# Optimization experiments

Measured on AMD Instinct MI355X. Metric: run time of the kernel, lower is better.

Reference implementation:

```python
import jax, jax.numpy as jnp
import numpy as np

N = 50000      # nodes
E = 800000     # edges (before self-loops)
F_IN = 256
H = 4          # heads
C1 = 128
C2 = 64
NCLS = 50
NEG_SLOPE = 0.2


def setup_inputs() -> dict:
    key = jax.random.key(0)
    ks = jax.random.split(key, 12)
    x = jax.random.normal(ks[0], (N, F_IN), dtype=jnp.float32)
    edge_index = jax.random.randint(ks[1], (2, E), 0, N, dtype=jnp.int32)
    s1 = 1.0 / np.sqrt(F_IN)
    s2 = 1.0 / np.sqrt(H * C1)
    s3 = 1.0 / np.sqrt(H * C2)
    return {
        "x": x,
        "edge_index": edge_index,
        "W1": jax.random.normal(ks[2], (F_IN, H * C1), dtype=jnp.float32) * s1,
        "a_src1": jax.random.normal(ks[3], (H, C1), dtype=jnp.float32) * s2,
        "a_dst1": jax.random.normal(ks[4], (H, C1), dtype=jnp.float32) * s2,
        "b1": jnp.zeros((H * C1,), dtype=jnp.float32),
        "W2": jax.random.normal(ks[5], (H * C1, H * C2), dtype=jnp.float32) * s2,
        "a_src2": jax.random.normal(ks[6], (H, C2), dtype=jnp.float32) * s3,
        "a_dst2": jax.random.normal(ks[7], (H, C2), dtype=jnp.float32) * s3,
        "b2": jnp.zeros((H * C2,), dtype=jnp.float32),
        "Wf": jax.random.normal(ks[8], (H * C2, NCLS), dtype=jnp.float32) * s3,
        "bf": jnp.zeros((NCLS,), dtype=jnp.float32),
    }


def _gat_conv(x, src, dst, W, a_src, a_dst, b, heads, ch):
    # h: [N, H, C] transformed features
    h = (x @ W).reshape(N, heads, ch)
    # per-node attention halves (standard GAT decomposition, avoids per-edge d-dim gather for scores)
    asrc = jnp.sum(h * a_src[None], axis=-1)  # [N, H]
    adst = jnp.sum(h * a_dst[None], axis=-1)  # [N, H]
    e = jax.nn.leaky_relu(asrc[src] + adst[dst], NEG_SLOPE)  # [E, H]
    # softmax over edges sharing the same destination node
    m = jax.ops.segment_max(e, dst, num_segments=N)          # [N, H]
    ex = jnp.exp(e - m[dst])
    denom = jax.ops.segment_sum(ex, dst, num_segments=N)     # [N, H]
    alpha = ex / (denom[dst] + 1e-16)                        # [E, H]
    msg = h[src] * alpha[:, :, None]                         # [E, H, C]
    out = jax.ops.segment_sum(msg, dst, num_segments=N)      # [N, H, C]
    return out.reshape(N, heads * ch) + b


def reference(x, edge_index, W1, a_src1, a_dst1, b1, W2, a_src2, a_dst2, b2, Wf, bf):
    # PyG GATConv adds self-loops by default
    loops = jnp.arange(N, dtype=edge_index.dtype)
    src = jnp.concatenate([edge_index[0], loops])
    dst = jnp.concatenate([edge_index[1], loops])
    h = _gat_conv(x, src, dst, W1, a_src1, a_dst1, b1, H, C1)
    h = jax.nn.elu(h)
    # F.dropout is identity in eval mode
    h = _gat_conv(h, src, dst, W2, a_src2, a_dst2, b2, H, C2)
    h = jax.nn.elu(h)
    return h @ Wf + bf
```

## Files before the change

kernel.cpp:

```cpp
#include <hip/hip_runtime.h>
#include <hip/hip_fp16.h>
#include <cmath>

#define NN 50000
#define EE 800000
#define ET 850000
#define HH 4
#define CC1 128
#define CC2 64
#define FIN 256
#define NCLS 50

typedef _Float16 half8_t __attribute__((ext_vector_type(8)));
typedef __attribute__((ext_vector_type(4))) float floatx4;

typedef const __attribute__((address_space(1))) unsigned int* glds_gp_t;
typedef __attribute__((address_space(3))) unsigned int* glds_lp_t;
__device__ __forceinline__ void glds16(const void* g, void* l) {
    __builtin_amdgcn_global_load_lds((glds_gp_t)g, (glds_lp_t)l, 16, 0, 0);
}

#define NB_CAST 12500
#define NB_W1   512
#define NB_W2   512
#define NB_WF   64
#define NB_VA   1
#define NB_HIST 3321
__global__ __launch_bounds__(256) void prep_hist(
    const float* __restrict__ x, __half* __restrict__ xb,
    const float* __restrict__ W1, __half* __restrict__ W1t,
    const float* __restrict__ W2, __half* __restrict__ W2t,
    const float* __restrict__ Wf, __half* __restrict__ Wft,
    const float* __restrict__ a_src1, const float* __restrict__ a_dst1,
    float* __restrict__ va, float* __restrict__ vd,
    const int* __restrict__ ei, int* __restrict__ deg)
{
    int b = blockIdx.x;
    if (b < NB_CAST) {
        int t = b * 256 + threadIdx.x;
        float4 v = *(const float4*)(x + 4 * (size_t)t);
        __half2 p[2];
        p[0] = __floats2half2_rn(v.x, v.y);
        p[1] = __floats2half2_rn(v.z, v.w);
        *(uint2*)(xb + 4 * (size_t)t) = *(uint2*)p;
    } else if (b < NB_CAST + NB_W1) {
        int t = (b - NB_CAST) * 256 + threadIdx.x;
        int n = t >> 8, k = t & 255;
        W1t[t] = __float2half(W1[(size_t)k * 512 + n]);
    } else if (b < NB_CAST + NB_W1 + NB_W2) {
        int t = (b - NB_CAST - NB_W1) * 256 + threadIdx.x;
        int n = t >> 9, k = t & 511;
        W2t[t] = __float2half(W2[(size_t)k * 256 + n]);
    } else if (b < NB_CAST + NB_W1 + NB_W2 + NB_WF) {
        int t = (b - NB_CAST - NB_W1 - NB_W2) * 256 + threadIdx.x;
        int n = t >> 8, k = t & 255;
        Wft[t] = (n < NCLS) ? __float2half(Wf[(size_t)k * NCLS + n]) : __float2half(0.f);
    } else if (b < NB_CAST + NB_W1 + NB_W2 + NB_WF + NB_VA) {
        int k = threadIdx.x;
        const float* wrow = W1 + (size_t)k * 512;
        float s1[4], s2[4];
        #pragma unroll
        for (int h = 0; h < 4; ++h) {
            float a1 = 0.f, a2 = 0.f;
            for (int c = 0; c < 128; ++c) {
                float w = wrow[h * 128 + c];
                a1 += w * a_src1[h * 128 + c];
                a2 += w * a_dst1[h * 128 + c];
            }
            s1[h] = a1; s2[h] = a2;
        }
        *(float4*)(va + 4 * k) = make_float4(s1[0], s1[1], s1[2], s1[3]);
        *(float4*)(vd + 4 * k) = make_float4(s2[0], s2[1], s2[2], s2[3]);
    } else {
        int t = (b - NB_CAST - NB_W1 - NB_W2 - NB_WF - NB_VA) * 256 + threadIdx.x;
        if (t < ET) {
            int dst = (t < EE) ? ei[EE + t] : (t - EE);
            atomicAdd(&deg[dst], 1);
        }
    }
}

#define SCAN_NB 25
__global__ __launch_bounds__(256) void scan_fused(
    const int* __restrict__ deg, int* __restrict__ off, int* __restrict__ pos)
{
    __shared__ int ws[4];
    __shared__ int base_s;
    int tid = threadIdx.x;
    int lane = tid & 63, wid = tid >> 6;

    int lim = blockIdx.x * 2048;
    int s0 = 0;
    for (int i = tid; i < lim; i += 256) s0 += deg[i];
    #pragma unroll
    for (int o = 32; o > 0; o >>= 1) s0 += __shfl_xor(s0, o, 64);
    if (lane == 0) ws[wid] = s0;
    __syncthreads();
    if (tid == 0) base_s = ws[0] + ws[1] + ws[2] + ws[3];
    __syncthreads();
    int base = base_s;
    __syncthreads();

    int i0 = blockIdx.x * 2048 + tid * 8;
    int v[8]; int s = 0;
    #pragma unroll
    for (int k = 0; k < 8; ++k) {
        int i = i0 + k;
        v[k] = (i < NN) ? deg[i] : 0;
        s += v[k];
    }
    int sc = s;
    #pragma unroll
    for (int o = 1; o < 64; o <<= 1) {
        int t = __shfl_up(sc, o, 64);
        if (lane >= o) sc += t;
    }
    if (lane == 63) ws[wid] = sc;
    __syncthreads();
    int woff = base;
    for (int w = 0; w < wid; ++w) woff += ws[w];
    int excl = woff + sc - s;
    #pragma unroll
    for (int k = 0; k < 8; ++k) {
        int i = i0 + k;
        if (i < NN) { off[i] = excl; pos[i] = excl; }
        excl += v[k];
    }
    if (blockIdx.x == 0 && tid == 0) off[NN] = ET;
}

__global__ void edge_scatter(const int* __restrict__ ei,
                             int* __restrict__ pos, int* __restrict__ csr_src)
{
    int t = blockIdx.x * blockDim.x + threadIdx.x;
    if (t >= ET) return;
    int src, dst;
    if (t < EE) { src = ei[t]; dst = ei[EE + t]; }
    else        { src = t - EE; dst = t - EE; }
    int p = atomicAdd(&pos[dst], 1);
    csr_src[p] = src;
}

__global__ __launch_bounds__(256) void attn1x(
    const __half* __restrict__ xb, const float* __restrict__ va,
    const float* __restrict__ vd, float* __restrict__ asrc,
    float* __restrict__ adst)
{
    int wave = threadIdx.x >> 6;
    int lane = threadIdx.x & 63;
    int n = blockIdx.x * 4 + wave;
    if (n >= NN) return;
    int k0 = lane * 4;
    union { uint2 u; __half2 h2[2]; } X;
    X.u = *(const uint2*)(xb + (size_t)n * 256 + k0);
    float xv[4];
    float2 f0 = __half22float2(X.h2[0]);
    float2 f1 = __half22float2(X.h2[1]);
    xv[0] = f0.x; xv[1] = f0.y; xv[2] = f1.x; xv[3] = f1.y;

    float s1[4] = {0.f, 0.f, 0.f, 0.f};
    float s2[4] = {0.f, 0.f, 0.f, 0.f};
    #pragma unroll
    for (int j = 0; j < 4; ++j) {
        float4 a = *(const float4*)(va + 4 * (k0 + j));
        float4 d = *(const float4*)(vd + 4 * (k0 + j));
        s1[0] += xv[j] * a.x; s1[1] += xv[j] * a.y;
        s1[2] += xv[j] * a.z; s1[3] += xv[j] * a.w;
        s2[0] += xv[j] * d.x; s2[1] += xv[j] * d.y;
        s2[2] += xv[j] * d.z; s2[3] += xv[j] * d.w;
    }
    #pragma unroll
    for (int o = 32; o > 0; o >>= 1) {
        #pragma unroll
        for (int h = 0; h < 4; ++h) {
            s1[h] += __shfl_xor(s1[h], o, 64);
            s2[h] += __shfl_xor(s2[h], o, 64);
        }
    }
    if (lane == 0) {
        *(float4*)(asrc + (size_t)n * HH) = make_float4(s1[0], s1[1], s1[2], s1[3]);
        *(float4*)(adst + (size_t)n * HH) = make_float4(s2[0], s2[1], s2[2], s2[3]);
    }
}

__global__ __launch_bounds__(256) void aggregate_x(
    const __half* __restrict__ xb, const int* __restrict__ off,
    const int* __restrict__ csr_src, const float* __restrict__ asrc,
    const float* __restrict__ adst, __half* __restrict__ xagg)
{
    constexpr int UNR = 8;
    __shared__ unsigned int exlds_all[4][64 * 4];
    int wave = threadIdx.x >> 6;
    int lane = threadIdx.x & 63;
    int n = blockIdx.x * 4 + wave;
    if (n >= NN) return;
    unsigned int* exlds = exlds_all[wave];
    int coff = lane * 4;

    int start = off[n], end = off[n + 1];
    float4 advv = *(const float4*)(adst + (size_t)n * HH);
    float dh0 = 0.f, dh1 = 0.f, dh2 = 0.f, dh3 = 0.f;
    __half2 acc2[4][2] = {};

    for (int cb = start; cb < end; cb += 64) {
        int eidx = cb + lane;
        bool valid = eidx < end;
        int s_lane = csr_src[valid ? eidx : end - 1];
        float4 t = *(const float4*)(asrc + (size_t)s_lane * HH);
        float e0 = t.x + advv.x; e0 = e0 > 0.f ? e0 : 0.2f * e0;
        float e1 = t.y + advv.y; e1 = e1 > 0.f ? e1 : 0.2f * e1;
        float e2 = t.z + advv.z; e2 = e2 > 0.f ? e2 : 0.2f * e2;
        float e3 = t.w + advv.w; e3 = e3 > 0.f ? e3 : 0.2f * e3;
        float x0 = valid ? __expf(e0) : 0.f;
        float x1 = valid ? __expf(e1) : 0.f;
        float x2 = valid ? __expf(e2) : 0.f;
        float x3 = valid ? __expf(e3) : 0.f;
        dh0 += x0; dh1 += x1; dh2 += x2; dh3 += x3;
        __half2 xp[4];
        xp[0] = __float2half2_rn(x0);
        xp[1] = __float2half2_rn(x1);
        xp[2] = __float2half2_rn(x2);
        xp[3] = __float2half2_rn(x3);
        *(uint4*)&exlds[lane * 4] = *(uint4*)xp;

        int cnt = end - cb; if (cnt > 64) cnt = 64;
        int jmax = (cnt + UNR - 1) & ~(UNR - 1);
        for (int jj = 0; jj < jmax; jj += UNR) {
            int sidx[UNR]; uint2 uv[UNR];
            #pragma unroll
            for (int u = 0; u < UNR; ++u) {
                sidx[u] = __builtin_amdgcn_readlane(s_lane, jj + u);
                uv[u] = *(const uint2*)(xb + (size_t)sidx[u] * 256 + coff);
            }
            #pragma unroll
            for (int u = 0; u < UNR; ++u) {
                union { uint4 q; __half2 h2[4]; } X;
                X.q = *(const uint4*)&exlds[(jj + u) * 4];
                union { uint2 q; __half2 h2[2]; } V;
                V.q = uv[u];
                #pragma unroll
                for (int h = 0; h < 4; ++h) {
                    acc2[h][0] = __hfma2(X.h2[h], V.h2[0], acc2[h][0]);
                    acc2[h][1] = __hfma2(X.h2[h], V.h2[1], acc2[h][1]);
                }
            }
        }
    }

    #pragma unroll
    for (int o = 32; o > 0; o >>= 1) {
        dh0 += __shfl_xor(dh0, o, 64);
        dh1 += __shfl_xor(dh1, o, 64);
        dh2 += __shfl_xor(dh2, o, 64);
        dh3 += __shfl_xor(dh3, o, 64);
    }
    float invh[4];
    invh[0] = 1.f / (dh0 + 1e-16f);
    invh[1] = 1.f / (dh1 + 1e-16f);
    invh[2] = 1.f / (dh2 + 1e-16f);
    invh[3] = 1.f / (dh3 + 1e-16f);
    #pragma unroll
    for (int h = 0; h < 4; ++h) {
        float2 f0 = __half22float2(acc2[h][0]);
        float2 f1 = __half22float2(acc2[h][1]);
        __half2 pk[2];
        pk[0] = __floats2half2_rn(f0.x * invh[h], f0.y * invh[h]);
        pk[1] = __floats2half2_rn(f1.x * invh[h], f1.y * invh[h]);
        *(uint2*)(xagg + (size_t)n * 1024 + h * 256 + coff) = *(uint2*)pk;
    }
}

__global__ __launch_bounds__(256) void gemm1e(
    const __half* __restrict__ xagg,
    const __half* __restrict__ W1t,
    const float* __restrict__ b1,
    __half* __restrict__ C, int M)
{
    __shared__ __half As[128 * 32];
    __shared__ __half Bs[128 * 32];
    int tid = threadIdx.x, wave = tid >> 6, lane = tid & 63;
    int wm = (wave >> 1) * 64, wn = (wave & 1) * 64;
    int row0 = blockIdx.x * 128, col0 = blockIdx.y * 128;
    int head = blockIdx.y;
    int lm = lane & 15, lq = lane >> 4, kq = lq * 8;
    floatx4 acc[4][4] = {};

    int srow = wave * 32 + (lane >> 2);
    int skk  = (lane & 3) * 8;
    int gra0 = row0 + srow;      if (gra0 >= M) gra0 = M - 1;
    int gra1 = row0 + srow + 16; if (gra1 >= M) gra1 = M - 1;
    const __half* ga0 = xagg + (size_t)gra0 * 1024 + head * 256 + skk;
    const __half* ga1 = xagg + (size_t)gra1 * 1024 + head * 256 + skk;
    const __half* gb0 = W1t + (size_t)(col0 + srow) * 256 + skk;
    const __half* gb1 = W1t + (size_t)(col0 + srow + 16) * 256 + skk;
    __half* la0 = &As[(wave * 32) * 32];
    __half* la1 = &As[(wave * 32 + 16) * 32];
    __half* lb0 = &Bs[(wave * 32) * 32];
    __half* lb1 = &Bs[(wave * 32 + 16) * 32];

    for (int k0 = 0; k0 < 256; k0 += 32) {
        __syncthreads();
        glds16(ga0 + k0, la0);
        glds16(ga1 + k0, la1);
        glds16(gb0 + k0, lb0);
        glds16(gb1 + k0, lb1);
        __syncthreads();

        half8_t af[4], bfr[4];
        #pragma unroll
        for (int mt = 0; mt < 4; ++mt)
            af[mt] = *(const half8_t*)&As[(wm + mt * 16 + lm) * 32 + kq];
        #pragma unroll
        for (int nt = 0; nt < 4; ++nt)
            bfr[nt] = *(const half8_t*)&Bs[(wn + nt * 16 + lm) * 32 + kq];
        #pragma unroll
        for (int mt = 0; mt < 4; ++mt)
            #pragma unroll
            for (int nt = 0; nt < 4; ++nt)
                acc[mt][nt] = __builtin_amdgcn_mfma_f32_16x16x32_f16(
                    af[mt], bfr[nt], acc[mt][nt], 0, 0, 0);
    }

    #pragma unroll
    for (int mt = 0; mt < 4; ++mt) {
        int rbase = row0 + wm + mt * 16 + lq * 4;
        #pragma unroll
        for (int nt = 0; nt < 4; ++nt) {
            int c = col0 + wn + nt * 16 + lm;
            float bv = b1[c];
            #pragma unroll
            for (int r = 0; r < 4; ++r) {
                int gr = rbase + r;
                if (gr < M) {
                    float v = acc[mt][nt][r] + bv;
                    v = v > 0.f ? v : expm1f(v);
                    C[(size_t)gr * 512 + c] = __float2half(v);
                }
            }
        }
    }
}

__global__ __launch_bounds__(256) void gemm_f16_v2(
    const __half* __restrict__ A,
    const __half* __restrict__ Bt,
    __half* __restrict__ C,
    int M, int N, int K)
{
    __shared__ __half As[128 * 32];
    __shared__ __half Bs[128 * 32];
    int tid = threadIdx.x, wave = tid >> 6, lane = tid & 63;
    int wm = (wave >> 1) * 64, wn = (wave & 1) * 64;
    int row0 = blockIdx.x * 128, col0 = blockIdx.y * 128;
    int lm = lane & 15, lq = lane >> 4, kq = lq * 8;
    floatx4 acc[4][4] = {};

    int srow = wave * 32 + (lane >> 2);
    int skk  = (lane & 3) * 8;
    int gra0 = row0 + srow;      if (gra0 >= M) gra0 = M - 1;
    int gra1 = row0 + srow + 16; if (gra1 >= M) gra1 = M - 1;
    const __half* ga0 = A + (size_t)gra0 * K + skk;
    const __half* ga1 = A + (size_t)gra1 * K + skk;
    const __half* gb0 = Bt + (size_t)(col0 + srow) * K + skk;
    const __half* gb1 = Bt + (size_t)(col0 + srow + 16) * K + skk;
    __half* la0 = &As[(wave * 32) * 32];
    __half* la1 = &As[(wave * 32 + 16) * 32];
    __half* lb0 = &Bs[(wave * 32) * 32];
    __half* lb1 = &Bs[(wave * 32 + 16) * 32];

    for (int k0 = 0; k0 < K; k0 += 32) {
        __syncthreads();
        glds16(ga0 + k0, la0);
        glds16(ga1 + k0, la1);
        glds16(gb0 + k0, lb0);
        glds16(gb1 + k0, lb1);
        __syncthreads();

        half8_t af[4], bfr[4];
        #pragma unroll
        for (int mt = 0; mt < 4; ++mt)
            af[mt] = *(const half8_t*)&As[(wm + mt * 16 + lm) * 32 + kq];
        #pragma unroll
        for (int nt = 0; nt < 4; ++nt)
            bfr[nt] = *(const half8_t*)&Bs[(wn + nt * 16 + lm) * 32 + kq];
        #pragma unroll
        for (int mt = 0; mt < 4; ++mt)
            #pragma unroll
            for (int nt = 0; nt < 4; ++nt)
                acc[mt][nt] = __builtin_amdgcn_mfma_f32_16x16x32_f16(
                    af[mt], bfr[nt], acc[mt][nt], 0, 0, 0);
    }

    #pragma unroll
    for (int mt = 0; mt < 4; ++mt) {
        int rbase = row0 + wm + mt * 16 + lq * 4;
        #pragma unroll
        for (int nt = 0; nt < 4; ++nt) {
            int c = col0 + wn + nt * 16 + lm;
            #pragma unroll
            for (int r = 0; r < 4; ++r) {
                int gr = rbase + r;
                if (gr < M) C[(size_t)gr * N + c] = __float2half(acc[mt][nt][r]);
            }
        }
    }
}

__global__ __launch_bounds__(128) void gemm_final(
    const __half* __restrict__ A,
    const __half* __restrict__ Bt,
    const float* __restrict__ bias,
    float* __restrict__ out, int M)
{
    __shared__ __half As[128 * 40];
    __shared__ __half Bs[64 * 40];
    int tid = threadIdx.x, wave = tid >> 6, lane = tid & 63;
    int row0 = blockIdx.x * 128;
    int lm = lane & 15, lq = lane >> 4, kq = lq * 8;
    floatx4 acc[4][4] = {};

    for (int k0 = 0; k0 < 256; k0 += 32) {
        int gr = row0 + tid; if (gr >= M) gr = M - 1;
        const __half* ap = A + (size_t)gr * 256 + k0;
        half8_t a0 = *(const half8_t*)ap;
        half8_t a1 = *(const half8_t*)(ap + 8);
        half8_t a2 = *(const half8_t*)(ap + 16);
        half8_t a3 = *(const half8_t*)(ap + 24);
        const __half* bp = Bt + (size_t)(tid >> 1) * 256 + k0 + (tid & 1) * 16;
        half8_t b0 = *(const half8_t*)bp;
        half8_t b1 = *(const half8_t*)(bp + 8);
        __syncthreads();
        *(half8_t*)&As[tid * 40 + 0]  = a0;
        *(half8_t*)&As[tid * 40 + 8]  = a1;
        *(half8_t*)&As[tid * 40 + 16] = a2;
        *(half8_t*)&As[tid * 40 + 24] = a3;
        *(half8_t*)&Bs[(tid >> 1) * 40 + (tid & 1) * 16]     = b0;
        *(half8_t*)&Bs[(tid >> 1) * 40 + (tid & 1) * 16 + 8] = b1;
        __syncthreads();

        half8_t af[4], bfr[4];
        #pragma unroll
        for (int mt = 0; mt < 4; ++mt)
            af[mt] = *(const half8_t*)&As[(wave * 64 + mt * 16 + lm) * 40 + kq];
        #pragma unroll
        for (int nt = 0; nt < 4; ++nt)
            bfr[nt] = *(const half8_t*)&Bs[(nt * 16 + lm) * 40 + kq];
        #pragma unroll
        for (int mt = 0; mt < 4; ++mt)
            #pragma unroll
            for (int nt = 0; nt < 4; ++nt)
                acc[mt][nt] = __builtin_amdgcn_mfma_f32_16x16x32_f16(
                    af[mt], bfr[nt], acc[mt][nt], 0, 0, 0);
    }

    #pragma unroll
    for (int mt = 0; mt < 4; ++mt) {
        int rbase = row0 + wave * 64 + mt * 16 + lq * 4;
        #pragma unroll
        for (int nt = 0; nt < 4; ++nt) {
            int c = nt * 16 + lm;
            if (c >= NCLS) continue;
            float bv = bias[c];
            #pragma unroll
            for (int r = 0; r < 4; ++r) {
                int gr = rbase + r;
                if (gr < M) out[(size_t)gr * NCLS + c] = acc[mt][nt][r] + bv;
            }
        }
    }
}

template<int C>
__global__ __launch_bounds__(256) void attn_scores2(
    const __half* __restrict__ h, const float* __restrict__ a_src,
    const float* __restrict__ a_dst, float* __restrict__ asrc,
    float* __restrict__ adst)
{
    constexpr int HC = HH * C;
    constexpr int CPL = HC / 64;
    int wave = threadIdx.x >> 6;
    int lane = threadIdx.x & 63;
    int n = blockIdx.x * 4 + wave;
    if (n >= NN) return;
    int c0 = lane * CPL;
    int head = c0 / C;
    const __half* hp = h + (size_t)n * HC + c0;
    float hv[CPL];
    union { uint2 u; __half2 h2[2]; } U;
    U.u = *(const uint2*)hp;
    #pragma unroll
    for (int k = 0; k < 2; ++k) {
        float2 f = __half22float2(U.h2[k]);
        hv[2 * k] = f.x; hv[2 * k + 1] = f.y;
    }
    float s1 = 0.f, s2 = 0.f;
    #pragma unroll
    for (int c = 0; c < CPL; ++c) {
        s1 += hv[c] * a_src[c0 + c];
        s2 += hv[c] * a_dst[c0 + c];
    }
    #pragma unroll
    for (int o = 8; o > 0; o >>= 1) {
        s1 += __shfl_xor(s1, o, 64);
        s2 += __shfl_xor(s2, o, 64);
    }
    if ((lane & 15) == 0) {
        asrc[n * HH + head] = s1;
        adst[n * HH + head] = s2;
    }
}

template<int C>
__global__ __launch_bounds__(256) void aggregate7(
    const __half* __restrict__ h, const int* __restrict__ off,
    const int* __restrict__ csr_src, const float* __restrict__ asrc,
    const float* __restrict__ adst, const float* __restrict__ bias,
    __half* __restrict__ outb)
{
    constexpr int HC = HH * C;
    constexpr int LPE = HC / 8;
    constexpr int EPW = 64 / LPE;
    constexpr int UNR = 8;
    __shared__ unsigned int exlds_all[4][64 * HH];
    int wave = threadIdx.x >> 6;
    int lane = threadIdx.x & 63;
    int n = blockIdx.x * 4 + wave;
    if (n >= NN) return;
    unsigned int* exlds = exlds_all[wave];
    int el  = (EPW == 1) ? 0 : (lane >> 5);
    int lel = (EPW == 1) ? lane : (lane & 31);
    int coff = lel * 8;
    int hl = coff / C;

    int start = off[n], end = off[n + 1];
    float4 advv = *(const float4*)(adst + (size_t)n * HH);
    float dh0 = 0.f, dh1 = 0.f, dh2 = 0.f, dh3 = 0.f;
    __half2 acc2[4] = {};

    for (int cb = start; cb < end; cb += 64) {
        int eidx = cb + lane;
        bool valid = eidx < end;
        int s_lane = csr_src[valid ? eidx : end - 1];
        float4 t = *(const float4*)(asrc + (size_t)s_lane * HH);
        float e0 = t.x + advv.x; e0 = e0 > 0.f ? e0 : 0.2f * e0;
        float e1 = t.y + advv.y; e1 = e1 > 0.f ? e1 : 0.2f * e1;
        float e2 = t.z + advv.z; e2 = e2 > 0.f ? e2 : 0.2f * e2;
        float e3 = t.w + advv.w; e3 = e3 > 0.f ? e3 : 0.2f * e3;
        float x0 = valid ? __expf(e0) : 0.f;
        float x1 = valid ? __expf(e1) : 0.f;
        float x2 = valid ? __expf(e2) : 0.f;
        float x3 = valid ? __expf(e3) : 0.f;
        dh0 += x0; dh1 += x1; dh2 += x2; dh3 += x3;
        __half2 xp[4];
        xp[0] = __float2half2_rn(x0);
        xp[1] = __float2half2_rn(x1);
        xp[2] = __float2half2_rn(x2);
        xp[3] = __float2half2_rn(x3);
        *(uint4*)&exlds[lane * 4] = *(uint4*)xp;

        int cnt = end - cb; if (cnt > 64) cnt = 64;
        int jmax = (cnt + UNR * EPW - 1) & ~(UNR * EPW - 1);
        for (int jj = 0; jj < jmax; jj += UNR * EPW) {
            int sidx[UNR]; __half2 xs[UNR];
            union { uint4 u; __half2 h2[4]; } uv[UNR];
            #pragma unroll
            for (int u = 0; u < UNR; ++u) {
                int e_lo = jj + u * EPW;
                int sa = __builtin_amdgcn_readlane(s_lane, e_lo);
                int sb = __builtin_amdgcn_readlane(s_lane, e_lo + 1);
                sidx[u] = el ? sb : sa;
                uv[u].u = *(const uint4*)(h + (size_t)sidx[u] * HC + coff);
                xs[u] = *(__half2*)&exlds[(e_lo + el) * 4 + hl];
            }
            #pragma unroll
            for (int u = 0; u < UNR; ++u)
                #pragma unroll
                for (int k = 0; k < 4; ++k)
                    acc2[k] = __hfma2(xs[u], uv[u].h2[k], acc2[k]);
        }
    }

    #pragma unroll
    for (int o = 32; o > 0; o >>= 1) {
        dh0 += __shfl_xor(dh0, o, 64);
        dh1 += __shfl_xor(dh1, o, 64);
        dh2 += __shfl_xor(dh2, o, 64);
        dh3 += __shfl_xor(dh3, o, 64);
    }
    float accf[8];
    #pragma unroll
    for (int k = 0; k < 4; ++k) {
        float2 f = __half22float2(acc2[k]);
        accf[2 * k] = f.x; accf[2 * k + 1] = f.y;
    }
    #pragma unroll
    for (int c = 0; c < 8; ++c)
        accf[c] += __shfl_xor(accf[c], 32, 64);
    float d = (hl == 0) ? dh0 : (hl == 1) ? dh1 : (hl == 2) ? dh2 : dh3;
    float inv = 1.f / (d + 1e-16f);
    if (el == 0) {
        float4 b0 = *(const float4*)(bias + coff);
        float4 b1 = *(const float4*)(bias + coff + 4);
        float bb[8] = {b0.x, b0.y, b0.z, b0.w, b1.x, b1.y, b1.z, b1.w};
        __half2 pk[4];
        #pragma unroll
        for (int c2 = 0; c2 < 4; ++c2) {
            float ua = accf[2 * c2]     * inv + bb[2 * c2];
            float ub = accf[2 * c2 + 1] * inv + bb[2 * c2 + 1];
            ua = ua > 0.f ? ua : expm1f(ua);
            ub = ub > 0.f ? ub : expm1f(ub);
            pk[c2] = __floats2half2_rn(ua, ub);
        }
        *(uint4*)(outb + (size_t)n * HC + coff) = *(uint4*)pk;
    }
}

extern "C" void kernel_launch(void* const* d_in, const int* in_sizes, int n_in,
                              void* d_out, int out_size, void* d_ws, size_t ws_size,
                              hipStream_t stream) {
    const float* x      = (const float*)d_in[0];
    const int*   ei     = (const int*)d_in[1];
    const float* W1     = (const float*)d_in[2];
    const float* a_src1 = (const float*)d_in[3];
    const float* a_dst1 = (const float*)d_in[4];
    const float* b1     = (const float*)d_in[5];
    const float* W2     = (const float*)d_in[6];
    const float* a_src2 = (const float*)d_in[7];
    const float* a_dst2 = (const float*)d_in[8];
    const float* b2     = (const float*)d_in[9];
    const float* Wf     = (const float*)d_in[10];
    const float* bf     = (const float*)d_in[11];
    float* out = (float*)d_out;

    char* p = (char*)d_ws;
    __half* xb    = (__half*)p; p += (size_t)NN * FIN * 2;
    __half* xagg  = (__half*)p; p += (size_t)NN * 1024 * 2;
    __half* out1b = (__half*)p; p += (size_t)NN * HH * CC1 * 2;
    __half* h2b   = (__half*)p; p += (size_t)NN * HH * CC2 * 2;
    __half* out2b = (__half*)p; p += (size_t)NN * HH * CC2 * 2;
    __half* W1t   = (__half*)p; p += (size_t)FIN * HH * CC1 * 2;
    __half* W2t   = (__half*)p; p += (size_t)HH * CC1 * HH * CC2 * 2;
    __half* Wft   = (__half*)p; p += (size_t)64 * HH * CC2 * 2;
    float* va     = (float*)p;  p += (size_t)FIN * HH * 4;
    float* vd     = (float*)p;  p += (size_t)FIN * HH * 4;
    float* asrc   = (float*)p;  p += (size_t)NN * HH * 4;
    float* adst   = (float*)p;  p += (size_t)NN * HH * 4;
    int* deg      = (int*)p;    p += (size_t)NN * 4;
    int* csr_off  = (int*)p;    p += (size_t)(NN + 1) * 4 + 12;
    int* csr_pos  = (int*)p;    p += (size_t)NN * 4;
    int* csr_src  = (int*)p;    p += (size_t)ET * 4;

    hipMemsetAsync(deg, 0, NN * sizeof(int), stream);

    prep_hist<<<NB_CAST + NB_W1 + NB_W2 + NB_WF + NB_VA + NB_HIST, 256, 0, stream>>>(
        x, xb, W1, W1t, W2, W2t, Wf, Wft, a_src1, a_dst1, va, vd, ei, deg);

    scan_fused<<<SCAN_NB, 256, 0, stream>>>(deg, csr_off, csr_pos);
    edge_scatter<<<(ET + 255) / 256, 256, 0, stream>>>(ei, csr_pos, csr_src);

    attn1x<<<(NN + 3) / 4, 256, 0, stream>>>(xb, va, vd, asrc, adst);
    aggregate_x<<<(NN + 3) / 4, 256, 0, stream>>>(xb, csr_off, csr_src, asrc, adst, xagg);
    gemm1e<<<dim3((NN + 127) / 128, 4), 256, 0, stream>>>(xagg, W1t, b1, out1b, NN);

    gemm_f16_v2<<<dim3((NN + 127) / 128, (HH * CC2) / 128), 256, 0, stream>>>(
        out1b, W2t, h2b, NN, HH * CC2, HH * CC1);
    attn_scores2<CC2><<<(NN + 3) / 4, 256, 0, stream>>>(h2b, a_src2, a_dst2, asrc, adst);
    aggregate7<CC2><<<(NN + 3) / 4, 256, 0, stream>>>(h2b, csr_off, csr_src, asrc, adst, b2, out2b);

    gemm_final<<<(NN + 127) / 128, 128, 0, stream>>>(out2b, Wft, bf, out, NN);
}
```

Before: 505.8 us.

## Fuse attention-score computation into x cast and second GEMM epilogue

Layer-1 attention scores are now computed inside the x-to-fp16 cast blocks of prep_hist, using va/vd from a new tiny kernel launched beforehand. This removes the separate attn1x pass that re-read xb. Layer-2 scores are computed in the epilogue of the second GEMM from the fp32 accumulators, which removes attn_scores2 and its re-read of h2b. The cost is one extra small kernel launch, a serial dependency of prep_hist on vavd, and some extra register pressure in the GEMM epilogue.

Result: no change. 510.0 us (+0.8%).

```diff
diff --git a/kernel.cpp b/kernel.cpp
--- a/kernel.cpp
+++ b/kernel.cpp
@@ -20,29 +20,76 @@
     __builtin_amdgcn_global_load_lds((glds_gp_t)g, (glds_lp_t)l, 16, 0, 0);
 }
 
+__global__ __launch_bounds__(256) void vavd_kernel(
+    const float* __restrict__ W1, const float* __restrict__ a_src1,
+    const float* __restrict__ a_dst1, float* __restrict__ va,
+    float* __restrict__ vd)
+{
+    int k = threadIdx.x;
+    const float* wrow = W1 + (size_t)k * 512;
+    float s1[4], s2[4];
+    #pragma unroll
+    for (int h = 0; h < 4; ++h) {
+        float a1 = 0.f, a2 = 0.f;
+        for (int c = 0; c < 128; ++c) {
+            float w = wrow[h * 128 + c];
+            a1 += w * a_src1[h * 128 + c];
+            a2 += w * a_dst1[h * 128 + c];
+        }
+        s1[h] = a1; s2[h] = a2;
+    }
+    *(float4*)(va + 4 * k) = make_float4(s1[0], s1[1], s1[2], s1[3]);
+    *(float4*)(vd + 4 * k) = make_float4(s2[0], s2[1], s2[2], s2[3]);
+}
+
 #define NB_CAST 12500
 #define NB_W1   512
 #define NB_W2   512
 #define NB_WF   64
-#define NB_VA   1
 #define NB_HIST 3321
 __global__ __launch_bounds__(256) void prep_hist(
     const float* __restrict__ x, __half* __restrict__ xb,
     const float* __restrict__ W1, __half* __restrict__ W1t,
     const float* __restrict__ W2, __half* __restrict__ W2t,
     const float* __restrict__ Wf, __half* __restrict__ Wft,
-    const float* __restrict__ a_src1, const float* __restrict__ a_dst1,
-    float* __restrict__ va, float* __restrict__ vd,
+    const float* __restrict__ va, const float* __restrict__ vd,
+    float* __restrict__ asrc, float* __restrict__ adst,
     const int* __restrict__ ei, int* __restrict__ deg)
 {
     int b = blockIdx.x;
     if (b < NB_CAST) {
-        int t = b * 256 + threadIdx.x;
-        float4 v = *(const float4*)(x + 4 * (size_t)t);
+        int lane = threadIdx.x & 63;
+        int row = b * 4 + (threadIdx.x >> 6);
+        int k0 = lane * 4;
+        float4 v = *(const float4*)(x + (size_t)row * 256 + k0);
         __half2 p[2];
         p[0] = __floats2half2_rn(v.x, v.y);
         p[1] = __floats2half2_rn(v.z, v.w);
-        *(uint2*)(xb + 4 * (size_t)t) = *(uint2*)p;
+        *(uint2*)(xb + (size_t)row * 256 + k0) = *(uint2*)p;
+        float xv[4] = {v.x, v.y, v.z, v.w};
+        float s1[4] = {0.f, 0.f, 0.f, 0.f};
+        float s2[4] = {0.f, 0.f, 0.f, 0.f};
+        #pragma unroll
+        for (int j = 0; j < 4; ++j) {
+            float4 a = *(const float4*)(va + 4 * (k0 + j));
+            float4 d = *(const float4*)(vd + 4 * (k0 + j));
+            s1[0] += xv[j] * a.x; s1[1] += xv[j] * a.y;
+            s1[2] += xv[j] * a.z; s1[3] += xv[j] * a.w;
+            s2[0] += xv[j] * d.x; s2[1] += xv[j] * d.y;
+            s2[2] += xv[j] * d.z; s2[3] += xv[j] * d.w;
+        }
+        #pragma unroll
+        for (int o = 32; o > 0; o >>= 1) {
+            #pragma unroll
+            for (int h = 0; h < 4; ++h) {
+                s1[h] += __shfl_xor(s1[h], o, 64);
+                s2[h] += __shfl_xor(s2[h], o, 64);
+            }
+        }
+        if (lane == 0) {
+            *(float4*)(asrc + (size_t)row * HH) = make_float4(s1[0], s1[1], s1[2], s1[3]);
+            *(float4*)(adst + (size_t)row * HH) = make_float4(s2[0], s2[1], s2[2], s2[3]);
+        }
     } else if (b < NB_CAST + NB_W1) {
         int t = (b - NB_CAST) * 256 + threadIdx.x;
         int n = t >> 8, k = t & 255;
@@ -55,24 +102,8 @@
         int t = (b - NB_CAST - NB_W1 - NB_W2) * 256 + threadIdx.x;
         int n = t >> 8, k = t & 255;
         Wft[t] = (n < NCLS) ? __float2half(Wf[(size_t)k * NCLS + n]) : __float2half(0.f);
-    } else if (b < NB_CAST + NB_W1 + NB_W2 + NB_WF + NB_VA) {
-        int k = threadIdx.x;
-        const float* wrow = W1 + (size_t)k * 512;
-        float s1[4], s2[4];
-        #pragma unroll
-        for (int h = 0; h < 4; ++h) {
-            float a1 = 0.f, a2 = 0.f;
-            for (int c = 0; c < 128; ++c) {
-                float w = wrow[h * 128 + c];
-                a1 += w * a_src1[h * 128 + c];
-                a2 += w * a_dst1[h * 128 + c];
-            }
-            s1[h] = a1; s2[h] = a2;
-        }
-        *(float4*)(va + 4 * k) = make_float4(s1[0], s1[1], s1[2], s1[3]);
-        *(float4*)(vd + 4 * k) = make_float4(s2[0], s2[1], s2[2], s2[3]);
     } else {
-        int t = (b - NB_CAST - NB_W1 - NB_W2 - NB_WF - NB_VA) * 256 + threadIdx.x;
+        int t = (b - NB_CAST - NB_W1 - NB_W2 - NB_WF) * 256 + threadIdx.x;
         if (t < ET) {
             int dst = (t < EE) ? ei[EE + t] : (t - EE);
             atomicAdd(&deg[dst], 1);
@@ -139,48 +170,6 @@
     else        { src = t - EE; dst = t - EE; }
     int p = atomicAdd(&pos[dst], 1);
     csr_src[p] = src;
-}
-
-__global__ __launch_bounds__(256) void attn1x(
-    const __half* __restrict__ xb, const float* __restrict__ va,
-    const float* __restrict__ vd, float* __restrict__ asrc,
-    float* __restrict__ adst)
-{
-    int wave = threadIdx.x >> 6;
-    int lane = threadIdx.x & 63;
-    int n = blockIdx.x * 4 + wave;
-    if (n >= NN) return;
-    int k0 = lane * 4;
-    union { uint2 u; __half2 h2[2]; } X;
-    X.u = *(const uint2*)(xb + (size_t)n * 256 + k0);
-    float xv[4];
-    float2 f0 = __half22float2(X.h2[0]);
-    float2 f1 = __half22float2(X.h2[1]);
-    xv[0] = f0.x; xv[1] = f0.y; xv[2] = f1.x; xv[3] = f1.y;
-
-    float s1[4] = {0.f, 0.f, 0.f, 0.f};
-    float s2[4] = {0.f, 0.f, 0.f, 0.f};
-    #pragma unroll
-    for (int j = 0; j < 4; ++j) {
-        float4 a = *(const float4*)(va + 4 * (k0 + j));
-        float4 d = *(const float4*)(vd + 4 * (k0 + j));
-        s1[0] += xv[j] * a.x; s1[1] += xv[j] * a.y;
-        s1[2] += xv[j] * a.z; s1[3] += xv[j] * a.w;
-        s2[0] += xv[j] * d.x; s2[1] += xv[j] * d.y;
-        s2[2] += xv[j] * d.z; s2[3] += xv[j] * d.w;
-    }
-    #pragma unroll
-    for (int o = 32; o > 0; o >>= 1) {
-        #pragma unroll
-        for (int h = 0; h < 4; ++h) {
-            s1[h] += __shfl_xor(s1[h], o, 64);
-            s2[h] += __shfl_xor(s2[h], o, 64);
-        }
-    }
-    if (lane == 0) {
-        *(float4*)(asrc + (size_t)n * HH) = make_float4(s1[0], s1[1], s1[2], s1[3]);
-        *(float4*)(adst + (size_t)n * HH) = make_float4(s2[0], s2[1], s2[2], s2[3]);
-    }
 }
 
 __global__ __launch_bounds__(256) void aggregate_x(
@@ -341,12 +330,16 @@
     }
 }
 
-__global__ __launch_bounds__(256) void gemm_f16_v2(
+__global__ __launch_bounds__(256) void gemm2s(
     const __half* __restrict__ A,
     const __half* __restrict__ Bt,
     __half* __restrict__ C,
-    int M, int N, int K)
-{
+    const float* __restrict__ a_src_full,
+    const float* __restrict__ a_dst_full,
+    float* __restrict__ asrc, float* __restrict__ adst,
+    int M)
+{
+    const int N = 256, K = 512;
     __shared__ __half As[128 * 32];
     __shared__ __half Bs[128 * 32];
     int tid = threadIdx.x, wave = tid >> 6, lane = tid & 63;
@@ -401,6 +394,35 @@
             for (int r = 0; r < 4; ++r) {
                 int gr = rbase + r;
                 if (gr < M) C[(size_t)gr * N + c] = __float2half(acc[mt][nt][r]);
+            }
+        }
+    }
+
+    float asw[4], adw[4];
+    #pragma unroll
+    for (int nt = 0; nt < 4; ++nt) {
+        int c = col0 + wn + nt * 16 + lm;
+        asw[nt] = a_src_full[c];
+        adw[nt] = a_dst_full[c];
+    }
+    int head = (col0 + wn) >> 6;
+    #pragma unroll
+    for (int mt = 0; mt < 4; ++mt) {
+        #pragma unroll
+        for (int r = 0; r < 4; ++r) {
+            float s1 = acc[mt][0][r] * asw[0] + acc[mt][1][r] * asw[1]
+                     + acc[mt][2][r] * asw[2] + acc[mt][3][r] * asw[3];
+            float s2 = acc[mt][0][r] * adw[0] + acc[mt][1][r] * adw[1]
+                     + acc[mt][2][r] * adw[2] + acc[mt][3][r] * adw[3];
+            #pragma unroll
+            for (int o = 1; o < 16; o <<= 1) {
+                s1 += __shfl_xor(s1, o, 64);
+                s2 += __shfl_xor(s2, o, 64);
+            }
+            int row = row0 + wm + mt * 16 + lq * 4 + r;
+            if (lm == 0 && row < M) {
+                asrc[row * HH + head] = s1;
+                adst[row * HH + head] = s2;
             }
         }
     }
@@ -467,46 +489,6 @@
                 if (gr < M) out[(size_t)gr * NCLS + c] = acc[mt][nt][r] + bv;
             }
         }
-    }
-}
-
-template<int C>
-__global__ __launch_bounds__(256) void attn_scores2(
-    const __half* __restrict__ h, const float* __restrict__ a_src,
-    const float* __restrict__ a_dst, float* __restrict__ asrc,
-    float* __restrict__ adst)
-{
-    constexpr int HC = HH * C;
-    constexpr int CPL = HC / 64;
-    int wave = threadIdx.x >> 6;
-    int lane = threadIdx.x & 63;
-    int n = blockIdx.x * 4 + wave;
-    if (n >= NN) return;
-    int c0 = lane * CPL;
-    int head = c0 / C;
-    const __half* hp = h + (size_t)n * HC + c0;
-    float hv[CPL];
-    union { uint2 u; __half2 h2[2]; } U;
-    U.u = *(const uint2*)hp;
-    #pragma unroll
-    for (int k = 0; k < 2; ++k) {
-        float2 f = __half22float2(U.h2[k]);
-        hv[2 * k] = f.x; hv[2 * k + 1] = f.y;
-    }
-    float s1 = 0.f, s2 = 0.f;
-    #pragma unroll
-    for (int c = 0; c < CPL; ++c) {
-        s1 += hv[c] * a_src[c0 + c];
-        s2 += hv[c] * a_dst[c0 + c];
-    }
-    #pragma unroll
-    for (int o = 8; o > 0; o >>= 1) {
-        s1 += __shfl_xor(s1, o, 64);
-        s2 += __shfl_xor(s2, o, 64);
-    }
-    if ((lane & 15) == 0) {
-        asrc[n * HH + head] = s1;
-        adst[n * HH + head] = s2;
     }
 }
 
@@ -652,19 +634,19 @@
 
     hipMemsetAsync(deg, 0, NN * sizeof(int), stream);
 
-    prep_hist<<<NB_CAST + NB_W1 + NB_W2 + NB_WF + NB_VA + NB_HIST, 256, 0, stream>>>(
-        x, xb, W1, W1t, W2, W2t, Wf, Wft, a_src1, a_dst1, va, vd, ei, deg);
+    vavd_kernel<<<1, 256, 0, stream>>>(W1, a_src1, a_dst1, va, vd);
+
+    prep_hist<<<NB_CAST + NB_W1 + NB_W2 + NB_WF + NB_HIST, 256, 0, stream>>>(
+        x, xb, W1, W1t, W2, W2t, Wf, Wft, va, vd, asrc, adst, ei, deg);
 
     scan_fused<<<SCAN_NB, 256, 0, stream>>>(deg, csr_off, csr_pos);
     edge_scatter<<<(ET + 255) / 256, 256, 0, stream>>>(ei, csr_pos, csr_src);
 
-    attn1x<<<(NN + 3) / 4, 256, 0, stream>>>(xb, va, vd, asrc, adst);
     aggregate_x<<<(NN + 3) / 4, 256, 0, stream>>>(xb, csr_off, csr_src, asrc, adst, xagg);
     gemm1e<<<dim3((NN + 127) / 128, 4), 256, 0, stream>>>(xagg, W1t, b1, out1b, NN);
 
-    gemm_f16_v2<<<dim3((NN + 127) / 128, (HH * CC2) / 128), 256, 0, stream>>>(
-        out1b, W2t, h2b, NN, HH * CC2, HH * CC1);
-    attn_scores2<CC2><<<(NN + 3) / 4, 256, 0, stream>>>(h2b, a_src2, a_dst2, asrc, adst);
+    gemm2s<<<dim3((NN + 127) / 128, 2), 256, 0, stream>>>(
+        out1b, W2t, h2b, a_src2, a_dst2, asrc, adst, NN);
     aggregate7<CC2><<<(NN + 3) / 4, 256, 0, stream>>>(h2b, csr_off, csr_src, asrc, adst, b2, out2b);
 
     gemm_final<<<(NN + 127) / 128, 128, 0, stream>>>(out2b, Wft, bf, out, NN);
```
